# Performance work log

Hardware: AMD Instinct MI355X
Metric: run time of the kernel (lower is better)

Reference implementation:

```python
import jax, jax.numpy as jnp
import numpy as np

N = 30000      # nodes
E = 400000     # edges per sparse set / GAT graph
F_IN = 512     # num_features
NHID = 128     # nhid
H = 4          # GAT heads
NCLS = 10      # num_classes
NSETS = 5      # num_gat = (3**2-1)//2 + 1
EPS = 1e-5     # BatchNorm eps


def setup_inputs() -> dict:
    key = jax.random.key(0)
    ks = jax.random.split(key, 24)
    s_in = 1.0 / np.sqrt(F_IN)
    s_h = 1.0 / np.sqrt(NHID)
    s_hh = 1.0 / np.sqrt(H * NHID)
    inp = {
        "x": jax.random.normal(ks[0], (N, F_IN), jnp.float32),
        "edge_index": jax.random.randint(ks[1], (2, E), 0, N),
        "scatter_idx": jax.random.randint(ks[2], (NSETS, 2, E), 0, N),
        "scatter_w": jax.random.normal(ks[3], (NSETS, E), jnp.float32) * 0.1,
        "lin_in_W": jax.random.normal(ks[4], (F_IN, NHID), jnp.float32) * s_in,
        "lin_in_b": jnp.zeros((NHID,), jnp.float32),
        "gat_W": jax.random.normal(ks[5], (NSETS, NHID, H * NHID), jnp.float32) * s_h,
        "att_src": jax.random.normal(ks[6], (NSETS, H, NHID), jnp.float32) * s_h,
        "att_dst": jax.random.normal(ks[7], (NSETS, H, NHID), jnp.float32) * s_h,
        "gat_b": jnp.zeros((NSETS, H * NHID), jnp.float32),
        "mlp_W": jax.random.normal(ks[8], (NSETS, H * NHID, NHID), jnp.float32) * s_hh,
        "mlp_b": jnp.zeros((NSETS, NHID), jnp.float32),
        "bn_g": jnp.ones((NSETS, NHID), jnp.float32),
        "bn_b": jnp.zeros((NSETS, NHID), jnp.float32),
        "bn_m": jax.random.normal(ks[9], (NSETS, NHID), jnp.float32) * 0.1,
        "bn_v": jax.random.uniform(ks[10], (NSETS, NHID), jnp.float32) + 0.5,
        "bn0_g": jnp.ones((NHID,), jnp.float32),
        "bn0_b": jnp.zeros((NHID,), jnp.float32),
        "bn0_m": jax.random.normal(ks[11], (NHID,), jnp.float32) * 0.1,
        "bn0_v": jax.random.uniform(ks[12], (NHID,), jnp.float32) + 0.5,
        "out_W": jax.random.normal(ks[13], (NHID, NCLS), jnp.float32) * s_h,
        "out_b": jnp.zeros((NCLS,), jnp.float32),
    }
    return inp


def _forward(x, edge_index, scatter_idx, scatter_w, lin_in_W, lin_in_b,
             gat_W, att_src, att_dst, gat_b, mlp_W, mlp_b,
             bn_g, bn_b, bn_m, bn_v, bn0_g, bn0_b, bn0_m, bn0_v, out_W, out_b):
    # solo_pass: gather source features, weight by edge value, scatter-add at dest
    def sp(i, xx):
        msg = scatter_w[i][:, None] * xx[scatter_idx[i, 0]]          # [E, NHID]
        return jax.ops.segment_sum(msg, scatter_idx[i, 1], num_segments=N)

    h = x @ lin_in_W + lin_in_b                                       # [N, NHID]
    x0 = sp(0, h)
    xhs = [jnp.abs(sp(i, h)) for i in range(1, NSETS)]
    xs = [x0] + [sp(0, xh) for xh in xhs]

    # GATConv adds self-loops by default
    loops = jnp.arange(N)
    src = jnp.concatenate([edge_index[0], loops])
    dst = jnp.concatenate([edge_index[1], loops])

    def gat(i, xx):
        hh = (xx @ gat_W[i]).reshape(N, H, NHID)                      # [N,H,C]
        a_s = (hh * att_src[i]).sum(-1)                               # [N,H]
        a_d = (hh * att_dst[i]).sum(-1)                               # [N,H]
        e = jax.nn.leaky_relu(a_s[src] + a_d[dst], 0.2)               # [E+N,H]
        m = jax.ops.segment_max(e, dst, num_segments=N)
        ex = jnp.exp(e - m[dst])
        den = jax.ops.segment_sum(ex, dst, num_segments=N)
        alpha = ex / (den[dst] + 1e-16)                               # [E+N,H]
        out = jax.ops.segment_sum(alpha[:, :, None] * hh[src], dst, num_segments=N)
        return out.reshape(N, H * NHID) + gat_b[i]

    # Seq(ELU, Dropout(eval=no-op), Linear, BatchNorm1d(eval))
    def mlp(i, xx):
        z = jax.nn.elu(xx) @ mlp_W[i] + mlp_b[i]
        return (z - bn_m[i]) * jax.lax.rsqrt(bn_v[i] + EPS) * bn_g[i] + bn_b[i]

    outs = [mlp(i, gat(i, xs[i])) for i in range(NSETS)]
    x_stage2 = h + outs[0] + outs[1] + outs[2] + outs[3] + outs[4]

    z = (x_stage2 - bn0_m) * jax.lax.rsqrt(bn0_v + EPS) * bn0_g + bn0_b
    z = jax.nn.elu(z) @ out_W + out_b
    return jax.nn.log_softmax(z, axis=1)


def reference(x, edge_index, scatter_idx, scatter_w, lin_in_W, lin_in_b,
              gat_W, att_src, att_dst, gat_b, mlp_W, mlp_b,
              bn_g, bn_b, bn_m, bn_v, bn0_g, bn0_b, bn0_m, bn0_v, out_W, out_b):
    return _forward(x, edge_index, scatter_idx, scatter_w, lin_in_W, lin_in_b,
                    gat_W, att_src, att_dst, gat_b, mlp_W, mlp_b,
                    bn_g, bn_b, bn_m, bn_v, bn0_g, bn0_b, bn0_m, bn0_v, out_W, out_b)
```

## Files before the change

kernel.cpp:

```cpp
#include <hip/hip_runtime.h>
#include <cstdint>
#include <cstddef>

#define NN 30000
#define NE 400000
#define EG (NE + NN)
#define NSETS 5
#define NCLS 10
#define BN_EPS 1e-5f

#define NBKT 118
#define CHUNK 4096
#define NWG_SET 98
#define NWG_GAT 105
#define NWGMAX 105
#define NBLK_BIN (5 * NWG_SET + NWG_GAT)
#define NBLK_SORT (6 * NBKT)
#define LIN_B 469

typedef __bf16 bf16x8 __attribute__((ext_vector_type(8)));
typedef float  f32x4  __attribute__((ext_vector_type(4)));

constexpr size_t alg(size_t x) { return (x + 255) & ~size_t(255); }
constexpr size_t OFF_U1    = 0;
constexpr size_t OFF_HB    = OFF_U1   + alg((size_t)5 * NN * 128 * 2);
constexpr size_t OFF_X2    = OFF_HB   + alg((size_t)NN * 128 * 2);
constexpr size_t OFF_AGG   = OFF_X2   + alg((size_t)NN * 128 * 4);
constexpr size_t OFF_GOUT  = OFF_AGG  + alg((size_t)NN * 512 * 2);
constexpr size_t OFF_WT    = OFF_GOUT + alg((size_t)NN * 512 * 2);
constexpr size_t OFF_WATT  = OFF_WT   + alg((size_t)11 * 65536 * 2);
constexpr size_t OFF_OFF6  = OFF_WATT + alg((size_t)5 * 2 * 4 * 128 * 4);
constexpr size_t OFF_SPP   = OFF_OFF6 + alg((size_t)6 * (NN + 1) * 4);
constexpr size_t OFF_GSRC  = OFF_SPP  + alg((size_t)NSETS * NE * 8);
constexpr size_t OFF_CNT   = OFF_GSRC + alg((size_t)EG * 4);
constexpr size_t OFF_AS5   = OFF_CNT  + alg((size_t)12 * NN * 4);
constexpr size_t OFF_AD5   = OFF_AS5  + alg((size_t)5 * NN * 4 * 4);
constexpr size_t WS_NEED   = OFF_AD5  + alg((size_t)5 * NN * 4 * 4);

__device__ __forceinline__ float lrelu02(float v) { return v > 0.f ? v : 0.2f * v; }
__device__ __forceinline__ float eluf(float v)    { return v > 0.f ? v : __expf(v) - 1.f; }
__device__ __forceinline__ float bf2f(unsigned u) {
    union { unsigned i; float f; } c; c.i = u << 16; return c.f;
}
__device__ __forceinline__ unsigned short f2bf(float f) {
    union { float f; unsigned i; } c; c.f = f;
    unsigned u = c.i + 0x7FFFu + ((c.i >> 16) & 1u);
    return (unsigned short)(u >> 16);
}
__device__ __forceinline__ void gload_lds16(const void* g, void* l) {
    __builtin_amdgcn_global_load_lds(
        (const __attribute__((address_space(1))) void*)(uintptr_t)g,
        (__attribute__((address_space(3))) void*)(unsigned)(uintptr_t)l,
        16, 0, 0);
}

__device__ __forceinline__ void chunk_map(int blk, int& g, int& wg, int& e0, int& e1) {
    if (blk < 5 * NWG_SET) { g = blk / NWG_SET; wg = blk - g * NWG_SET; }
    else                   { g = 5;             wg = blk - 5 * NWG_SET; }
    e0 = wg * CHUNK;
    e1 = min(e0 + CHUNK, (g < 5) ? NE : EG);
}

#define PREP_CVX_B 1024
#define PREP_TRW_B 512
#define PREP_WAT_B 20
#define PREP_HIST_B NBLK_BIN
#define PREP_GRID (PREP_CVX_B + PREP_TRW_B + PREP_WAT_B + PREP_HIST_B)

__global__ void prep1(const int* __restrict__ scat_idx, const int* __restrict__ edge_ix,
                      int* __restrict__ bh,
                      const float* __restrict__ x, unsigned short* __restrict__ xb,
                      const float* __restrict__ lin_W, const float* __restrict__ gat_W,
                      const float* __restrict__ mlp_W,
                      unsigned short* __restrict__ linWT, unsigned short* __restrict__ gatWT,
                      unsigned short* __restrict__ mlpWT,
                      const float* __restrict__ att_src, const float* __restrict__ att_dst,
                      float* __restrict__ watt) {
    __shared__ int h[NBKT];
    const int b = blockIdx.x;
    if (b < PREP_CVX_B) {
        const int total = NN * 512 / 4;
        for (int i = b * 256 + threadIdx.x; i < total; i += PREP_CVX_B * 256) {
            float4 v = *(const float4*)(x + (size_t)i * 4);
            ushort4 o;
            o.x = f2bf(v.x); o.y = f2bf(v.y); o.z = f2bf(v.z); o.w = f2bf(v.w);
            *(ushort4*)(xb + (size_t)i * 4) = o;
        }
    } else if (b < PREP_CVX_B + PREP_TRW_B) {
        const int bb = b - PREP_CVX_B;
        const int total = 65536 + 2 * 327680;
        for (int i = bb * 256 + threadIdx.x; i < total; i += PREP_TRW_B * 256) {
            if (i < 65536) {
                int n = i >> 9, k = i & 511;
                linWT[i] = f2bf(lin_W[(size_t)k * 128 + n]);
            } else if (i < 65536 + 327680) {
                int li = i - 65536;
                int st = li >> 16, r = li & 65535;
                int n = r >> 7, k = r & 127;
                gatWT[li] = f2bf(gat_W[(size_t)st * 65536 + (size_t)k * 512 + n]);
            } else {
                int li = i - 65536 - 327680;
// ... 157 lines not shown
        int g, wg, e0, e1;
        chunk_map(blockIdx.x - LIN_B, g, wg, e0, e1);
        for (int i = t; i < NBKT; i += 256) {
            lpos[i] = pos[(size_t)(g * NBKT + i) * NWGMAX + wg];
            lcur[i] = 0;
        }
        __syncthreads();
        if (g < 5) {
            const int* si = scat_idx + (size_t)g * 2 * NE;
            const float* sw = scat_w + (size_t)g * NE;
            for (int e = e0 + t; e < e1; e += 256) {
                int src = si[e], d = si[NE + e];
                int r = atomicAdd(&lcur[d >> 8], 1);
                int2 pk; pk.x = src | (d << 15); pk.y = __float_as_int(sw[e]);
                stg_sp[(size_t)g * NE + lpos[d >> 8] + r] = pk;
            }
        } else {
            for (int e = e0 + t; e < e1; e += 256) {
                int src, d;
                if (e < NE) { src = edge_ix[e]; d = edge_ix[NE + e]; }
                else        { src = e - NE;     d = src; }
                int r = atomicAdd(&lcur[d >> 8], 1);
                stg_g[lpos[d >> 8] + r] = src | (d << 15);
            }
        }
    }
}

__global__ void __launch_bounds__(256) sortP(const int* __restrict__ bb,
                                             const int2* __restrict__ stg_sp, const int* __restrict__ stg_g,
                                             int2* __restrict__ spp, int* __restrict__ g_src,
                                             int* __restrict__ off6) {
    __shared__ int lcnt[256];
    __shared__ int loff[257];
    const int gb = blockIdx.x;
    const int g = gb / NBKT, bk = gb - g * NBKT;
    const int n0 = bk << 8;
    const int nlen = min(256, NN - n0);
    const int base = bb[g * 132 + bk];
    const int end  = bb[g * 132 + bk + 1];
    const int t = threadIdx.x;
    lcnt[t] = 0;
    __syncthreads();
    if (g < 5) {
        for (int j = base + t; j < end; j += 256)
            atomicAdd(&lcnt[((stg_sp[(size_t)g * NE + j].x >> 15) & 0x7fff) - n0], 1);
    } else {
        for (int j = base + t; j < end; j += 256)
            atomicAdd(&lcnt[((stg_g[j] >> 15) & 0x7fff) - n0], 1);
    }
    __syncthreads();
    int v = lcnt[t];
    __syncthreads();
    for (int d = 1; d < 256; d <<= 1) {
        int u = (t >= d) ? lcnt[t - d] : 0;
        __syncthreads();
        lcnt[t] += u;
        __syncthreads();
    }
    loff[t] = base + lcnt[t] - v;
    if (t == 255) loff[256] = base + lcnt[255];
    __syncthreads();
    if (t < nlen) off6[g * (NN + 1) + n0 + t] = loff[t];
    lcnt[t] = 0;
    __syncthreads();
    if (g < 5) {
        for (int j = base + t; j < end; j += 256) {
            int2 pk = stg_sp[(size_t)g * NE + j];
            int ln = ((pk.x >> 15) & 0x7fff) - n0;
            int p = loff[ln] + atomicAdd(&lcnt[ln], 1);
            int2 o; o.x = pk.x & 0x7fff; o.y = pk.y;
            spp[(size_t)g * NE + p] = o;
        }
    } else {
        for (int j = base + t; j < end; j += 256) {
            int w = stg_g[j];
            int ln = ((w >> 15) & 0x7fff) - n0;
            int p = loff[ln] + atomicAdd(&lcnt[ln], 1);
            g_src[p] = w & 0x7fff;
        }
    }
}

__global__ void __launch_bounds__(256) fusedGM(const unsigned short* __restrict__ agg,
                                               const unsigned short* __restrict__ gatWT,
                                               const unsigned short* __restrict__ mlpWT,
                                               const float* __restrict__ gat_b,
                                               const float* __restrict__ mlp_b,
                                               const float* __restrict__ bng, const float* __restrict__ bnb,
                                               const float* __restrict__ bnm, const float* __restrict__ bnv,
                                               float* __restrict__ x2) {
    __shared__ __align__(16) char U[49152];
    __shared__ __align__(16) char gtile[16384];
    const int t = threadIdx.x, wave = t >> 6, lane = t & 63;
    const int bm = blockIdx.x * 64;
    const int wr = (wave >> 1) * 32, wc = (wave & 1) * 64;
    const int l15 = lane & 15, l4 = lane >> 4;
    const int rsw = (l15 & 7) << 4;
    f32x4 acc2[2][4] = {};

    #pragma unroll
    for (int h = 0; h < 4; ++h) {
        stage64<64>(agg, 512, bm, NN - 1, h * 128,       U,         t);
        stage64<64>(agg, 512, bm, NN - 1, h * 128 + 64,  U + 8192,  t);
        stage64<128>(gatWT, 128, h * 128, 511, 0,        U + 16384, t);
        stage64<128>(gatWT, 128, h * 128, 511, 64,       U + 32768, t);
        __syncthreads();

        f32x4 a1[2][4] = {};
        #pragma unroll
        for (int ks = 0; ks < 4; ++ks) {
            const char* Asb = U + (ks >> 1) * 8192;
            const char* Bsb = U + 16384 + (ks >> 1) * 16384;
            const int koff = (ks & 1) * 64 + l4 * 16;
            bf16x8 af[2], bf[4];
            #pragma unroll
            for (int fm = 0; fm < 2; ++fm)
                af[fm] = *(const bf16x8*)(Asb + (wr + fm * 16 + l15) * 128 + (koff ^ rsw));
            #pragma unroll
            for (int fn = 0; fn < 4; ++fn)
                bf[fn] = *(const bf16x8*)(Bsb + (wc + fn * 16 + l15) * 128 + (koff ^ rsw));
            #pragma unroll
            for (int fm = 0; fm < 2; ++fm)
                #pragma unroll
                for (int fn = 0; fn < 4; ++fn)
                    a1[fm][fn] = __builtin_amdgcn_mfma_f32_16x16x32_bf16(af[fm], bf[fn], a1[fm][fn], 0, 0, 0);
        }
        __syncthreads();

        #pragma unroll
        for (int fn = 0; fn < 4; ++fn) {
            const int cc = wc + fn * 16 + l15;
            const float gb = gat_b[h * 128 + cc];
            #pragma unroll
            for (int fm = 0; fm < 2; ++fm) {
                #pragma unroll
                for (int rg = 0; rg < 4; ++rg) {
                    const int r = wr + fm * 16 + l4 * 4 + rg;
                    const unsigned short v = f2bf(eluf(a1[fm][fn][rg] + gb));
                    *(unsigned short*)(gtile + r * 256 + ((((cc >> 3) ^ (r & 7)) << 4) | ((cc & 7) << 1))) = v;
                }
            }
        }
        stage64<128>(mlpWT, 512, 0, 127, h * 128,      U,         t);
        stage64<128>(mlpWT, 512, 0, 127, h * 128 + 64, U + 16384, t);
        __syncthreads();

        #pragma unroll
        for (int ks = 0; ks < 4; ++ks) {
            const int s2 = ks >> 1, kk = ks & 1;
            const char* slab = U + s2 * 16384;
            bf16x8 af[2], bf[4];
            #pragma unroll
            for (int fm = 0; fm < 2; ++fm) {
                const int r2 = wr + fm * 16 + l15;
                const int chunk = (s2 * 8 + kk * 4 + l4) ^ (r2 & 7);
                af[fm] = *(const bf16x8*)(gtile + r2 * 256 + (chunk << 4));
            }
            const int koff = kk * 64 + l4 * 16;
            #pragma unroll
            for (int fn = 0; fn < 4; ++fn)
                bf[fn] = *(const bf16x8*)(slab + (wc + fn * 16 + l15) * 128 + (koff ^ rsw));
            #pragma unroll
            for (int fm = 0; fm < 2; ++fm)
                #pragma unroll
                for (int fn = 0; fn < 4; ++fn)
                    acc2[fm][fn] = __builtin_amdgcn_mfma_f32_16x16x32_bf16(af[fm], bf[fn], acc2[fm][fn], 0, 0, 0);
        }
        __syncthreads();
    }

    #pragma unroll
    for (int fn = 0; fn < 4; ++fn) {
        const int c = wc + fn * 16 + l15;
        const float sc = bng[c] * rsqrtf(bnv[c] + BN_EPS);
        const float sh = bnb[c] - bnm[c] * sc;
        const float mb = mlp_b[c];
        #pragma unroll
        for (int fm = 0; fm < 2; ++fm) {
            #pragma unroll
            for (int rg = 0; rg < 4; ++rg) {
                int r = bm + wr + fm * 16 + l4 * 4 + rg;
                if (r < NN)
                    x2[(size_t)r * 128 + c] += (acc2[fm][fn][rg] + mb) * sc + sh;
            }
        }
    }
}

__global__ void __launch_bounds__(256) sp_abs4(const int* __restrict__ off6,
                                               const int2* __restrict__ spp,
                                               const unsigned short* __restrict__ hb,
                                               unsigned short* __restrict__ tmp4) {
    const int y = blockIdx.y;
    const int* off = off6 + (y + 1) * (NN + 1);
    const int2* pk = spp + (size_t)(y + 1) * NE;
    unsigned short* out = tmp4 + (size_t)y * NN * 128;

    const int wid  = blockIdx.x * 4 + (threadIdx.x >> 6);
    const int lane = threadIdx.x & 63;
    const int co   = lane * 2;
    const int s0 = off[wid], s1 = off[wid + 1];
    float a0 = 0.f, a1 = 0.f;
    int j = s0;
    for (; j + 7 < s1; j += 8) {
        int2 e[8];
        unsigned v[8];
        #pragma unroll
        for (int q = 0; q < 8; ++q) e[q] = pk[j + q];
        #pragma unroll
        for (int q = 0; q < 8; ++q) v[q] = *(const unsigned*)(hb + (size_t)e[q].x * 128 + co);
        #pragma unroll
        for (int q = 0; q < 8; ++q) {
            float w = __int_as_float(e[q].y);
            a0 = fmaf(w, bf2f(v[q] & 0xffffu), a0);
            a1 = fmaf(w, bf2f(v[q] >> 16), a1);
        }
    }
    for (; j < s1; ++j) {
        int2 e = pk[j];
        float wj = __int_as_float(e.y);
        unsigned v = *(const unsigned*)(hb + (size_t)e.x * 128 + co);
        a0 = fmaf(wj, bf2f(v & 0xffffu), a0);
        a1 = fmaf(wj, bf2f(v >> 16), a1);
    }
    a0 = fabsf(a0); a1 = fabsf(a1);
    unsigned o = (unsigned)f2bf(a0) | ((unsigned)f2bf(a1) << 16);
    *(unsigned*)(out + (size_t)wid * 128 + co) = o;
}

__global__ void __launch_bounds__(256) sp_fused5(const int* __restrict__ off0,
                                                 const int2* __restrict__ spp0,
                                                 const unsigned short* __restrict__ hb,
                                                 const unsigned short* __restrict__ tmp4,
                                                 unsigned short* __restrict__ xcur5,
                                                 const float* __restrict__ watt,
                                                 float* __restrict__ as5,
                                                 float* __restrict__ ad5) {
    __shared__ float sWatt[5120];
    for (int i = threadIdx.x; i < 5120; i += 256) sWatt[i] = watt[i];
    __syncthreads();

    const int wid  = blockIdx.x * 4 + (threadIdx.x >> 6);
    const int lane = threadIdx.x & 63;
    const int co   = lane * 2;
    const int s0 = off0[wid], s1 = off0[wid + 1];
    const unsigned short* tbl[5] = {
        hb, tmp4, tmp4 + (size_t)1 * NN * 128, tmp4 + (size_t)2 * NN * 128, tmp4 + (size_t)3 * NN * 128 };

    float a[5][2] = {};
    int j = s0;
    for (; j + 3 < s1; j += 4) {
        int2 e0 = spp0[j], e1 = spp0[j + 1], e2 = spp0[j + 2], e3 = spp0[j + 3];
        size_t r0 = (size_t)e0.x * 128 + co, r1 = (size_t)e1.x * 128 + co;
        size_t r2 = (size_t)e2.x * 128 + co, r3 = (size_t)e3.x * 128 + co;
        unsigned v[5][4];
        #pragma unroll
        for (int y = 0; y < 5; ++y) {
            v[y][0] = *(const unsigned*)(tbl[y] + r0);
            v[y][1] = *(const unsigned*)(tbl[y] + r1);
            v[y][2] = *(const unsigned*)(tbl[y] + r2);
            v[y][3] = *(const unsigned*)(tbl[y] + r3);
        }
        float w0 = __int_as_float(e0.y), w1 = __int_as_float(e1.y);
        float w2 = __int_as_float(e2.y), w3 = __int_as_float(e3.y);
        #pragma unroll
        for (int y = 0; y < 5; ++y) {
            a[y][0] = fmaf(w0, bf2f(v[y][0] & 0xffffu), a[y][0]); a[y][1] = fmaf(w0, bf2f(v[y][0] >> 16), a[y][1]);
            a[y][0] = fmaf(w1, bf2f(v[y][1] & 0xffffu), a[y][0]); a[y][1] = fmaf(w1, bf2f(v[y][1] >> 16), a[y][1]);
            a[y][0] = fmaf(w2, bf2f(v[y][2] & 0xffffu), a[y][0]); a[y][1] = fmaf(w2, bf2f(v[y][2] >> 16), a[y][1]);
            a[y][0] = fmaf(w3, bf2f(v[y][3] & 0xffffu), a[y][0]); a[y][1] = fmaf(w3, bf2f(v[y][3] >> 16), a[y][1]);
        }
    }
    for (; j < s1; ++j) {
        int2 e = spp0[j];
        size_t r = (size_t)e.x * 128 + co;
        float wj = __int_as_float(e.y);
        #pragma unroll
        for (int y = 0; y < 5; ++y) {
            unsigned v = *(const unsigned*)(tbl[y] + r);
            a[y][0] = fmaf(wj, bf2f(v & 0xffffu), a[y][0]);
            a[y][1] = fmaf(wj, bf2f(v >> 16), a[y][1]);
        }
    }
    #pragma unroll
    for (int y = 0; y < 5; ++y) {
        unsigned o = (unsigned)f2bf(a[y][0]) | ((unsigned)f2bf(a[y][1]) << 16);
        *(unsigned*)(xcur5 + (size_t)y * NN * 128 + (size_t)wid * 128 + co) = o;
    }

    #pragma unroll
    for (int i = 0; i < 5; ++i) {
        #pragma unroll
        for (int h = 0; h < 4; ++h) {
            const float* wS = sWatt + ((i * 2 + 0) * 4 + h) * 128;
            const float* wD = sWatt + ((i * 2 + 1) * 4 + h) * 128;
            float ps = a[i][0] * wS[co] + a[i][1] * wS[co + 1];
            float pd = a[i][0] * wD[co] + a[i][1] * wD[co + 1];
            #pragma unroll
            for (int dd = 1; dd < 64; dd <<= 1) { ps += __shfl_xor(ps, dd); pd += __shfl_xor(pd, dd); }
            if (lane == 0) {
                as5[(size_t)i * NN * 4 + (size_t)wid * 4 + h] = ps;
                ad5[(size_t)i * NN * 4 + (size_t)wid * 4 + h] = pd;
            }
        }
    }
}

__device__ __forceinline__ void acc8(float* a, float al, uint4 v) {
    a[0] = fmaf(al, bf2f(v.x & 0xffffu), a[0]); a[1] = fmaf(al, bf2f(v.x >> 16), a[1]);
    a[2] = fmaf(al, bf2f(v.y & 0xffffu), a[2]); a[3] = fmaf(al, bf2f(v.y >> 16), a[3]);
    a[4] = fmaf(al, bf2f(v.z & 0xffffu), a[4]); a[5] = fmaf(al, bf2f(v.z >> 16), a[5]);
    a[6] = fmaf(al, bf2f(v.w & 0xffffu), a[6]); a[7] = fmaf(al, bf2f(v.w >> 16), a[7]);
}

__global__ void __launch_bounds__(256) gat_agg2(const int* __restrict__ goff, const int* __restrict__ gsrc,
                                                const float* __restrict__ as_, const float* __restrict__ ad_,
                                                const unsigned short* __restrict__ xcur,
                                                unsigned short* __restrict__ agg) {
    const int wid  = blockIdx.x * 4 + (threadIdx.x >> 6);
    const int lane = threadIdx.x & 63;
    const int hd   = lane >> 4;
    const int cl   = (lane & 15) * 8;
    const int s0 = goff[wid], s1 = goff[wid + 1];
    const float4 adv4 = *(const float4*)(ad_ + (size_t)wid * 4);

    float m[4] = {-1e30f, -1e30f, -1e30f, -1e30f};
    float s[4] = {0.f, 0.f, 0.f, 0.f};
    for (int j = s0 + lane; j < s1; j += 64) {
        const int si = gsrc[j];
        float4 av = *(const float4*)(as_ + (size_t)si * 4);
        float e[4] = {lrelu02(av.x + adv4.x), lrelu02(av.y + adv4.y),
                      lrelu02(av.z + adv4.z), lrelu02(av.w + adv4.w)};
        #pragma unroll
        for (int h = 0; h < 4; ++h) {
            if (e[h] > m[h]) { s[h] = s[h] * __expf(m[h] - e[h]) + 1.f; m[h] = e[h]; }
            else             { s[h] += __expf(e[h] - m[h]); }
        }
    }
    #pragma unroll
    for (int d = 1; d < 64; d <<= 1) {
        #pragma unroll
        for (int h = 0; h < 4; ++h) {
            float om = __shfl_xor(m[h], d);
            float os = __shfl_xor(s[h], d);
            float nm = fmaxf(m[h], om);
            s[h] = s[h] * __expf(m[h] - nm) + os * __expf(om - nm);
            m[h] = nm;
        }
    }
    const float advh = hd == 0 ? adv4.x : hd == 1 ? adv4.y : hd == 2 ? adv4.z : adv4.w;
    const float mv   = hd == 0 ? m[0]   : hd == 1 ? m[1]   : hd == 2 ? m[2]   : m[3];
    const float dv   = hd == 0 ? s[0]   : hd == 1 ? s[1]   : hd == 2 ? s[2]   : s[3];
    const float inv  = 1.f / (dv + 1e-16f);

    float ac[8] = {};
    int j = s0;
    for (; j + 3 < s1; j += 4) {
        int i0 = gsrc[j], i1 = gsrc[j + 1], i2 = gsrc[j + 2], i3 = gsrc[j + 3];
        float q0 = as_[(size_t)i0 * 4 + hd], q1 = as_[(size_t)i1 * 4 + hd];
        float q2 = as_[(size_t)i2 * 4 + hd], q3 = as_[(size_t)i3 * 4 + hd];
        uint4 v0 = *(const uint4*)(xcur + (size_t)i0 * 128 + cl);
        uint4 v1 = *(const uint4*)(xcur + (size_t)i1 * 128 + cl);
        uint4 v2 = *(const uint4*)(xcur + (size_t)i2 * 128 + cl);
        uint4 v3 = *(const uint4*)(xcur + (size_t)i3 * 128 + cl);
        float al0 = __expf(lrelu02(q0 + advh) - mv) * inv;
        float al1 = __expf(lrelu02(q1 + advh) - mv) * inv;
        float al2 = __expf(lrelu02(q2 + advh) - mv) * inv;
        float al3 = __expf(lrelu02(q3 + advh) - mv) * inv;
        acc8(ac, al0, v0); acc8(ac, al1, v1); acc8(ac, al2, v2); acc8(ac, al3, v3);
    }
    for (; j < s1; ++j) {
        int si = gsrc[j];
        float q = as_[(size_t)si * 4 + hd];
        uint4 v = *(const uint4*)(xcur + (size_t)si * 128 + cl);
        float al = __expf(lrelu02(q + advh) - mv) * inv;
        acc8(ac, al, v);
    }
    uint4 ov;
    ov.x = (unsigned)f2bf(ac[0]) | ((unsigned)f2bf(ac[1]) << 16);
    ov.y = (unsigned)f2bf(ac[2]) | ((unsigned)f2bf(ac[3]) << 16);
    ov.z = (unsigned)f2bf(ac[4]) | ((unsigned)f2bf(ac[5]) << 16);
    ov.w = (unsigned)f2bf(ac[6]) | ((unsigned)f2bf(ac[7]) << 16);
    *(uint4*)(agg + (size_t)wid * 512 + hd * 128 + cl) = ov;
}

__global__ void __launch_bounds__(256) final_out(const float* __restrict__ x2,
                                                 const float* __restrict__ bn0g, const float* __restrict__ bn0b,
                                                 const float* __restrict__ bn0m, const float* __restrict__ bn0v,
                                                 const float* __restrict__ outW, const float* __restrict__ outb,
                                                 float* __restrict__ out) {
    __shared__ float sW[128 * 12];
    __shared__ float sSc[128], sSh[128];
    for (int i = threadIdx.x; i < 1280; i += 256) {
        int r = i / 10, c = i - r * 10;
        sW[r * 12 + c] = outW[i];
    }
    if (threadIdx.x < 128) {
        int c = threadIdx.x;
        float sc = bn0g[c] * rsqrtf(bn0v[c] + BN_EPS);
        sSc[c] = sc;
        sSh[c] = bn0b[c] - bn0m[c] * sc;
    }
    __syncthreads();
    const int wid  = blockIdx.x * 4 + (threadIdx.x >> 6);
    const int lane = threadIdx.x & 63;
    const int c0 = lane * 2;
    float2 a = *(const float2*)(x2 + (size_t)wid * 128 + c0);
    float a0 = eluf(a.x * sSc[c0] + sSh[c0]);
    float a1 = eluf(a.y * sSc[c0 + 1] + sSh[c0 + 1]);
    float p[NCLS];
    #pragma unroll
    for (int j = 0; j < NCLS; ++j)
        p[j] = a0 * sW[c0 * 12 + j] + a1 * sW[(c0 + 1) * 12 + j];
    #pragma unroll
    for (int j = 0; j < NCLS; ++j) {
        float v = p[j];
        v += __shfl_xor(v, 1);  v += __shfl_xor(v, 2);  v += __shfl_xor(v, 4);
        v += __shfl_xor(v, 8);  v += __shfl_xor(v, 16); v += __shfl_xor(v, 32);
        p[j] = v;
    }
    float z[NCLS];
    #pragma unroll
    for (int j = 0; j < NCLS; ++j) z[j] = p[j] + outb[j];
    float m = z[0];
    #pragma unroll
    for (int j = 1; j < NCLS; ++j) m = fmaxf(m, z[j]);
    float ssum = 0.f;
    #pragma unroll
    for (int j = 0; j < NCLS; ++j) ssum += __expf(z[j] - m);
    float lse = m + __logf(ssum);
    #pragma unroll
    for (int j = 0; j < NCLS; ++j)
        if (lane == j) out[(size_t)wid * NCLS + j] = z[j] - lse;
}

extern "C" void kernel_launch(void* const* d_in, const int* in_sizes, int n_in,
                              void* d_out, int out_size, void* d_ws, size_t ws_size,
                              hipStream_t stream) {
    const float* x        = (const float*)d_in[0];
    const int*   edge_ix  = (const int*)  d_in[1];
    const int*   scat_idx = (const int*)  d_in[2];
    const float* scat_w   = (const float*)d_in[3];
    const float* lin_W    = (const float*)d_in[4];
    const float* lin_b    = (const float*)d_in[5];
    const float* gat_W    = (const float*)d_in[6];
    const float* att_src  = (const float*)d_in[7];
    const float* att_dst  = (const float*)d_in[8];
    const float* gat_b    = (const float*)d_in[9];
    const float* mlp_W    = (const float*)d_in[10];
    const float* mlp_b    = (const float*)d_in[11];
    const float* bn_g     = (const float*)d_in[12];
    const float* bn_b     = (const float*)d_in[13];
    const float* bn_m     = (const float*)d_in[14];
    const float* bn_v     = (const float*)d_in[15];
    const float* bn0_g    = (const float*)d_in[16];
    const float* bn0_b    = (const float*)d_in[17];
    const float* bn0_m    = (const float*)d_in[18];
    const float* bn0_v    = (const float*)d_in[19];
    const float* out_W    = (const float*)d_in[20];
    const float* out_b    = (const float*)d_in[21];
    float* out = (float*)d_out;

    char* ws = (char*)d_ws;
    unsigned short* xb    = (unsigned short*)(ws + OFF_U1);
    unsigned short* xcur5 = (unsigned short*)(ws + OFF_U1);
    unsigned short* hb    = (unsigned short*)(ws + OFF_HB);
    float*          x2    = (float*)(ws + OFF_X2);
    unsigned short* agg   = (unsigned short*)(ws + OFF_AGG);
    unsigned short* tmp4  = (unsigned short*)(ws + OFF_GOUT);
    int2*  stg_sp = (int2*)(ws + OFF_GOUT);
    int*   stg_g  = (int*)(ws + OFF_GOUT + (size_t)NSETS * NE * 8);
    unsigned short* wt    = (unsigned short*)(ws + OFF_WT);
    unsigned short* linWT = wt;
    unsigned short* gatWT = wt + 65536;
    unsigned short* mlpWT = wt + 65536 * 6;
    float* watt   = (float*)(ws + OFF_WATT);
    int*   off6   = (int*)(ws + OFF_OFF6);
    int2*  spp    = (int2*)(ws + OFF_SPP);
    int*   g_src  = (int*)(ws + OFF_GSRC);
    int*   bh     = (int*)(ws + OFF_CNT);
    int*   bb     = bh + NBLK_SORT * NWGMAX;
    float* as5    = (float*)(ws + OFF_AS5);
    float* ad5    = (float*)(ws + OFF_AD5);

    const dim3 b256(256);

    prep1<<<PREP_GRID, b256, 0, stream>>>(scat_idx, edge_ix, bh, x, xb,
                                          lin_W, gat_W, mlp_W, linWT, gatWT, mlpWT,
                                          att_src, att_dst, watt);
    bktscan<<<6, 128, 0, stream>>>(bh, bb, off6);
    wgscan<<<NBLK_SORT, 128, 0, stream>>>(bb, bh);
    binlin<<<LIN_B + NBLK_BIN, b256, 0, stream>>>(scat_idx, scat_w, edge_ix, bh, stg_sp, stg_g,
                                                  xb, linWT, lin_b, hb, x2);
    sortP<<<NBLK_SORT, b256, 0, stream>>>(bb, stg_sp, stg_g, spp, g_src, off6);

    sp_abs4<<<dim3(7500, 4), b256, 0, stream>>>(off6, spp, hb, tmp4);
    sp_fused5<<<7500, b256, 0, stream>>>(off6, spp, hb, tmp4, xcur5, watt, as5, ad5);

    for (int i = 0; i < NSETS; ++i) {
        gat_agg2<<<7500, b256, 0, stream>>>(off6 + 5 * (NN + 1), g_src,
                                            as5 + (size_t)i * NN * 4, ad5 + (size_t)i * NN * 4,
                                            xcur5 + (size_t)i * NN * 128, agg);
        fusedGM<<<469, b256, 0, stream>>>(agg, gatWT + (size_t)i * 65536, mlpWT + (size_t)i * 65536,
                                          gat_b + (size_t)i * 512, mlp_b + (size_t)i * 128,
                                          bn_g + (size_t)i * 128, bn_b + (size_t)i * 128,
                                          bn_m + (size_t)i * 128, bn_v + (size_t)i * 128, x2);
    }

    final_out<<<7500, b256, 0, stream>>>(x2, bn0_g, bn0_b, bn0_m, bn0_v, out_W, out_b, out);
}
```

Baseline: 665.9 us.

## Overlap GAT aggregation of set i with GEMM+MLP of set i-1 in one kernel

Adds a combined kernel that runs the dense GAT-projection+MLP+BN work for the previous set alongside the sparse attention aggregation for the current set, using double-buffered aggregation outputs. The GEMM body is restructured to use less LDS (a smaller A/B staging buffer with more syncs) so the gather blocks and matrix blocks can co-reside on the same compute units. The goal is to hide the memory-bound gather latency behind MFMA work and cut kernel launches. In exchange there are more barriers in the GEMM, and the block-type dispatch by blockIdx can make the two kinds of blocks compete for resources.

Result: slower. 936.5 us (+40.6%).

```diff
diff --git a/kernel.cpp b/kernel.cpp
--- a/kernel.cpp
+++ b/kernel.cpp
@@ -17,6 +17,8 @@
 #define NBLK_BIN (5 * NWG_SET + NWG_GAT)
 #define NBLK_SORT (6 * NBKT)
 #define LIN_B 469
+#define GM_B 469
+#define COMB_GRID (GM_B * 17)
 
 typedef __bf16 bf16x8 __attribute__((ext_vector_type(8)));
 typedef float  f32x4  __attribute__((ext_vector_type(4)));
@@ -340,231 +342,6 @@
     }
 }
 
-__global__ void __launch_bounds__(256) fusedGM(const unsigned short* __restrict__ agg,
-                                               const unsigned short* __restrict__ gatWT,
-                                               const unsigned short* __restrict__ mlpWT,
-                                               const float* __restrict__ gat_b,
-                                               const float* __restrict__ mlp_b,
-                                               const float* __restrict__ bng, const float* __restrict__ bnb,
-                                               const float* __restrict__ bnm, const float* __restrict__ bnv,
-                                               float* __restrict__ x2) {
-    __shared__ __align__(16) char U[49152];
-    __shared__ __align__(16) char gtile[16384];
-    const int t = threadIdx.x, wave = t >> 6, lane = t & 63;
-    const int bm = blockIdx.x * 64;
-    const int wr = (wave >> 1) * 32, wc = (wave & 1) * 64;
-    const int l15 = lane & 15, l4 = lane >> 4;
-    const int rsw = (l15 & 7) << 4;
-    f32x4 acc2[2][4] = {};
-
-    #pragma unroll
-    for (int h = 0; h < 4; ++h) {
-        stage64<64>(agg, 512, bm, NN - 1, h * 128,       U,         t);
-        stage64<64>(agg, 512, bm, NN - 1, h * 128 + 64,  U + 8192,  t);
-        stage64<128>(gatWT, 128, h * 128, 511, 0,        U + 16384, t);
-        stage64<128>(gatWT, 128, h * 128, 511, 64,       U + 32768, t);
-        __syncthreads();
-
-        f32x4 a1[2][4] = {};
-        #pragma unroll
-        for (int ks = 0; ks < 4; ++ks) {
-            const char* Asb = U + (ks >> 1) * 8192;
-            const char* Bsb = U + 16384 + (ks >> 1) * 16384;
-            const int koff = (ks & 1) * 64 + l4 * 16;
-            bf16x8 af[2], bf[4];
-            #pragma unroll
-            for (int fm = 0; fm < 2; ++fm)
-                af[fm] = *(const bf16x8*)(Asb + (wr + fm * 16 + l15) * 128 + (koff ^ rsw));
-            #pragma unroll
-            for (int fn = 0; fn < 4; ++fn)
-                bf[fn] = *(const bf16x8*)(Bsb + (wc + fn * 16 + l15) * 128 + (koff ^ rsw));
-            #pragma unroll
-            for (int fm = 0; fm < 2; ++fm)
-                #pragma unroll
-                for (int fn = 0; fn < 4; ++fn)
-                    a1[fm][fn] = __builtin_amdgcn_mfma_f32_16x16x32_bf16(af[fm], bf[fn], a1[fm][fn], 0, 0, 0);
-        }
-        __syncthreads();
-
-        #pragma unroll
-        for (int fn = 0; fn < 4; ++fn) {
-            const int cc = wc + fn * 16 + l15;
-            const float gb = gat_b[h * 128 + cc];
-            #pragma unroll
-            for (int fm = 0; fm < 2; ++fm) {
-                #pragma unroll
-                for (int rg = 0; rg < 4; ++rg) {
-                    const int r = wr + fm * 16 + l4 * 4 + rg;
-                    const unsigned short v = f2bf(eluf(a1[fm][fn][rg] + gb));
-                    *(unsigned short*)(gtile + r * 256 + ((((cc >> 3) ^ (r & 7)) << 4) | ((cc & 7) << 1))) = v;
-                }
-            }
-        }
-        stage64<128>(mlpWT, 512, 0, 127, h * 128,      U,         t);
-        stage64<128>(mlpWT, 512, 0, 127, h * 128 + 64, U + 16384, t);
-        __syncthreads();
-
-        #pragma unroll
-        for (int ks = 0; ks < 4; ++ks) {
-            const int s2 = ks >> 1, kk = ks & 1;
-            const char* slab = U + s2 * 16384;
-            bf16x8 af[2], bf[4];
-            #pragma unroll
-            for (int fm = 0; fm < 2; ++fm) {
-                const int r2 = wr + fm * 16 + l15;
-                const int chunk = (s2 * 8 + kk * 4 + l4) ^ (r2 & 7);
-                af[fm] = *(const bf16x8*)(gtile + r2 * 256 + (chunk << 4));
-            }
-            const int koff = kk * 64 + l4 * 16;
-            #pragma unroll
-            for (int fn = 0; fn < 4; ++fn)
-                bf[fn] = *(const bf16x8*)(slab + (wc + fn * 16 + l15) * 128 + (koff ^ rsw));
-            #pragma unroll
-            for (int fm = 0; fm < 2; ++fm)
-                #pragma unroll
-                for (int fn = 0; fn < 4; ++fn)
-                    acc2[fm][fn] = __builtin_amdgcn_mfma_f32_16x16x32_bf16(af[fm], bf[fn], acc2[fm][fn], 0, 0, 0);
-        }
-        __syncthreads();
-    }
-
-    #pragma unroll
-    for (int fn = 0; fn < 4; ++fn) {
-        const int c = wc + fn * 16 + l15;
-        const float sc = bng[c] * rsqrtf(bnv[c] + BN_EPS);
-        const float sh = bnb[c] - bnm[c] * sc;
-        const float mb = mlp_b[c];
-        #pragma unroll
-        for (int fm = 0; fm < 2; ++fm) {
-            #pragma unroll
-            for (int rg = 0; rg < 4; ++rg) {
-                int r = bm + wr + fm * 16 + l4 * 4 + rg;
-                if (r < NN)
-                    x2[(size_t)r * 128 + c] += (acc2[fm][fn][rg] + mb) * sc + sh;
-            }
-        }
-    }
-}
-
-__global__ void __launch_bounds__(256) sp_abs4(const int* __restrict__ off6,
-                                               const int2* __restrict__ spp,
-                                               const unsigned short* __restrict__ hb,
-                                               unsigned short* __restrict__ tmp4) {
-    const int y = blockIdx.y;
-    const int* off = off6 + (y + 1) * (NN + 1);
-    const int2* pk = spp + (size_t)(y + 1) * NE;
-    unsigned short* out = tmp4 + (size_t)y * NN * 128;
-
-    const int wid  = blockIdx.x * 4 + (threadIdx.x >> 6);
-    const int lane = threadIdx.x & 63;
-    const int co   = lane * 2;
-    const int s0 = off[wid], s1 = off[wid + 1];
-    float a0 = 0.f, a1 = 0.f;
-    int j = s0;
-    for (; j + 7 < s1; j += 8) {
-        int2 e[8];
-        unsigned v[8];
-        #pragma unroll
-        for (int q = 0; q < 8; ++q) e[q] = pk[j + q];
-        #pragma unroll
-        for (int q = 0; q < 8; ++q) v[q] = *(const unsigned*)(hb + (size_t)e[q].x * 128 + co);
-        #pragma unroll
-        for (int q = 0; q < 8; ++q) {
-            float w = __int_as_float(e[q].y);
-            a0 = fmaf(w, bf2f(v[q] & 0xffffu), a0);
-            a1 = fmaf(w, bf2f(v[q] >> 16), a1);
-        }
-    }
-    for (; j < s1; ++j) {
-        int2 e = pk[j];
-        float wj = __int_as_float(e.y);
-        unsigned v = *(const unsigned*)(hb + (size_t)e.x * 128 + co);
-        a0 = fmaf(wj, bf2f(v & 0xffffu), a0);
-        a1 = fmaf(wj, bf2f(v >> 16), a1);
-    }
-    a0 = fabsf(a0); a1 = fabsf(a1);
-    unsigned o = (unsigned)f2bf(a0) | ((unsigned)f2bf(a1) << 16);
-    *(unsigned*)(out + (size_t)wid * 128 + co) = o;
-}
-
-__global__ void __launch_bounds__(256) sp_fused5(const int* __restrict__ off0,
-                                                 const int2* __restrict__ spp0,
-                                                 const unsigned short* __restrict__ hb,
-                                                 const unsigned short* __restrict__ tmp4,
-                                                 unsigned short* __restrict__ xcur5,
-                                                 const float* __restrict__ watt,
-                                                 float* __restrict__ as5,
-                                                 float* __restrict__ ad5) {
-    __shared__ float sWatt[5120];
-    for (int i = threadIdx.x; i < 5120; i += 256) sWatt[i] = watt[i];
-    __syncthreads();
-
-    const int wid  = blockIdx.x * 4 + (threadIdx.x >> 6);
-    const int lane = threadIdx.x & 63;
-    const int co   = lane * 2;
-    const int s0 = off0[wid], s1 = off0[wid + 1];
-    const unsigned short* tbl[5] = {
-        hb, tmp4, tmp4 + (size_t)1 * NN * 128, tmp4 + (size_t)2 * NN * 128, tmp4 + (size_t)3 * NN * 128 };
-
-    float a[5][2] = {};
-    int j = s0;
-    for (; j + 3 < s1; j += 4) {
-        int2 e0 = spp0[j], e1 = spp0[j + 1], e2 = spp0[j + 2], e3 = spp0[j + 3];
-        size_t r0 = (size_t)e0.x * 128 + co, r1 = (size_t)e1.x * 128 + co;
-        size_t r2 = (size_t)e2.x * 128 + co, r3 = (size_t)e3.x * 128 + co;
-        unsigned v[5][4];
-        #pragma unroll
-        for (int y = 0; y < 5; ++y) {
-            v[y][0] = *(const unsigned*)(tbl[y] + r0);
-            v[y][1] = *(const unsigned*)(tbl[y] + r1);
-            v[y][2] = *(const unsigned*)(tbl[y] + r2);
-            v[y][3] = *(const unsigned*)(tbl[y] + r3);
-        }
-        float w0 = __int_as_float(e0.y), w1 = __int_as_float(e1.y);
-        float w2 = __int_as_float(e2.y), w3 = __int_as_float(e3.y);
-        #pragma unroll
-        for (int y = 0; y < 5; ++y) {
-            a[y][0] = fmaf(w0, bf2f(v[y][0] & 0xffffu), a[y][0]); a[y][1] = fmaf(w0, bf2f(v[y][0] >> 16), a[y][1]);
-            a[y][0] = fmaf(w1, bf2f(v[y][1] & 0xffffu), a[y][0]); a[y][1] = fmaf(w1, bf2f(v[y][1] >> 16), a[y][1]);
-            a[y][0] = fmaf(w2, bf2f(v[y][2] & 0xffffu), a[y][0]); a[y][1] = fmaf(w2, bf2f(v[y][2] >> 16), a[y][1]);
-            a[y][0] = fmaf(w3, bf2f(v[y][3] & 0xffffu), a[y][0]); a[y][1] = fmaf(w3, bf2f(v[y][3] >> 16), a[y][1]);
-        }
-    }
-    for (; j < s1; ++j) {
-        int2 e = spp0[j];
-        size_t r = (size_t)e.x * 128 + co;
-        float wj = __int_as_float(e.y);
-        #pragma unroll
-        for (int y = 0; y < 5; ++y) {
-            unsigned v = *(const unsigned*)(tbl[y] + r);
-            a[y][0] = fmaf(wj, bf2f(v & 0xffffu), a[y][0]);
-            a[y][1] = fmaf(wj, bf2f(v >> 16), a[y][1]);
-        }
-    }
-    #pragma unroll
-    for (int y = 0; y < 5; ++y) {
-        unsigned o = (unsigned)f2bf(a[y][0]) | ((unsigned)f2bf(a[y][1]) << 16);
-        *(unsigned*)(xcur5 + (size_t)y * NN * 128 + (size_t)wid * 128 + co) = o;
-    }
-
-    #pragma unroll
-    for (int i = 0; i < 5; ++i) {
-        #pragma unroll
-        for (int h = 0; h < 4; ++h) {
-            const float* wS = sWatt + ((i * 2 + 0) * 4 + h) * 128;
-            const float* wD = sWatt + ((i * 2 + 1) * 4 + h) * 128;
-            float ps = a[i][0] * wS[co] + a[i][1] * wS[co + 1];
-            float pd = a[i][0] * wD[co] + a[i][1] * wD[co + 1];
-            #pragma unroll
-            for (int dd = 1; dd < 64; dd <<= 1) { ps += __shfl_xor(ps, dd); pd += __shfl_xor(pd, dd); }
-            if (lane == 0) {
-                as5[(size_t)i * NN * 4 + (size_t)wid * 4 + h] = ps;
-                ad5[(size_t)i * NN * 4 + (size_t)wid * 4 + h] = pd;
-            }
-        }
-    }
-}
-
 __device__ __forceinline__ void acc8(float* a, float al, uint4 v) {
     a[0] = fmaf(al, bf2f(v.x & 0xffffu), a[0]); a[1] = fmaf(al, bf2f(v.x >> 16), a[1]);
     a[2] = fmaf(al, bf2f(v.y & 0xffffu), a[2]); a[3] = fmaf(al, bf2f(v.y >> 16), a[3]);
@@ -572,14 +349,13 @@
     a[6] = fmaf(al, bf2f(v.w & 0xffffu), a[6]); a[7] = fmaf(al, bf2f(v.w >> 16), a[7]);
 }
 
-__global__ void __launch_bounds__(256) gat_agg2(const int* __restrict__ goff, const int* __restrict__ gsrc,
-                                                const float* __restrict__ as_, const float* __restrict__ ad_,
-                                                const unsigned short* __restrict__ xcur,
-                                                unsigned short* __restrict__ agg) {
-    const int wid  = blockIdx.x * 4 + (threadIdx.x >> 6);
-    const int lane = threadIdx.x & 63;
-    const int hd   = lane >> 4;
-    const int cl   = (lane & 15) * 8;
+__device__ __forceinline__ void gat_body(int wid, int lane,
+                                         const int* __restrict__ goff, const int* __restrict__ gsrc,
+                                         const float* __restrict__ as_, const float* __restrict__ ad_,
+                                         const unsigned short* __restrict__ xcur,
+                                         unsigned short* __restrict__ agg) {
+    const int hd = lane >> 4;
+    const int cl = (lane & 15) * 8;
     const int s0 = goff[wid], s1 = goff[wid + 1];
     const float4 adv4 = *(const float4*)(ad_ + (size_t)wid * 4);
 
@@ -641,6 +417,274 @@
     ov.z = (unsigned)f2bf(ac[4]) | ((unsigned)f2bf(ac[5]) << 16);
     ov.w = (unsigned)f2bf(ac[6]) | ((unsigned)f2bf(ac[7]) << 16);
     *(uint4*)(agg + (size_t)wid * 512 + hd * 128 + cl) = ov;
+}
+
+__global__ void __launch_bounds__(256) gat_agg2(const int* __restrict__ goff, const int* __restrict__ gsrc,
+                                                const float* __restrict__ as_, const float* __restrict__ ad_,
+                                                const unsigned short* __restrict__ xcur,
+                                                unsigned short* __restrict__ agg) {
+    gat_body(blockIdx.x * 4 + (threadIdx.x >> 6), threadIdx.x & 63, goff, gsrc, as_, ad_, xcur, agg);
+}
+
+__device__ __forceinline__ void gm40_body(int bm, int t, char* shm,
+                                          const unsigned short* __restrict__ agg,
+                                          const unsigned short* __restrict__ gatWT,
+                                          const unsigned short* __restrict__ mlpWT,
+                                          const float* __restrict__ gat_b,
+                                          const float* __restrict__ mlp_b,
+                                          const float* __restrict__ bng, const float* __restrict__ bnb,
+                                          const float* __restrict__ bnm, const float* __restrict__ bnv,
+                                          float* __restrict__ x2) {
+    char* Ab = shm;
+    char* Bb = shm + 8192;
+    char* gt = shm + 8192 + 16384;
+    const int wave = t >> 6, lane = t & 63;
+    const int wr = (wave >> 1) * 32, wc = (wave & 1) * 64;
+    const int l15 = lane & 15, l4 = lane >> 4;
+    const int rsw = (l15 & 7) << 4;
+    f32x4 acc2[2][4] = {};
+
+    #pragma unroll
+    for (int h = 0; h < 4; ++h) {
+        f32x4 a1[2][4] = {};
+        #pragma unroll
+        for (int ks2 = 0; ks2 < 2; ++ks2) {
+            stage64<64>(agg, 512, bm, NN - 1, h * 128 + ks2 * 64, Ab, t);
+            stage64<128>(gatWT, 128, h * 128, 511, ks2 * 64, Bb, t);
+            __syncthreads();
+            #pragma unroll
+            for (int kk = 0; kk < 2; ++kk) {
+                bf16x8 af[2], bf[4];
+                const int koff = kk * 64 + l4 * 16;
+                #pragma unroll
+                for (int fm = 0; fm < 2; ++fm)
+                    af[fm] = *(const bf16x8*)(Ab + (wr + fm * 16 + l15) * 128 + (koff ^ rsw));
+                #pragma unroll
+                for (int fn = 0; fn < 4; ++fn)
+                    bf[fn] = *(const bf16x8*)(Bb + (wc + fn * 16 + l15) * 128 + (koff ^ rsw));
+                #pragma unroll
+                for (int fm = 0; fm < 2; ++fm)
+                    #pragma unroll
+                    for (int fn = 0; fn < 4; ++fn)
+                        a1[fm][fn] = __builtin_amdgcn_mfma_f32_16x16x32_bf16(af[fm], bf[fn], a1[fm][fn], 0, 0, 0);
+            }
+            __syncthreads();
+        }
+        #pragma unroll
+        for (int fn = 0; fn < 4; ++fn) {
+            const int cc = wc + fn * 16 + l15;
+            const float gb = gat_b[h * 128 + cc];
+            #pragma unroll
+            for (int fm = 0; fm < 2; ++fm) {
+                #pragma unroll
+                for (int rg = 0; rg < 4; ++rg) {
+                    const int r = wr + fm * 16 + l4 * 4 + rg;
+                    const unsigned short v = f2bf(eluf(a1[fm][fn][rg] + gb));
+                    *(unsigned short*)(gt + r * 256 + ((((cc >> 3) ^ (r & 7)) << 4) | ((cc & 7) << 1))) = v;
+                }
+            }
+        }
+        #pragma unroll
+        for (int ks2 = 0; ks2 < 2; ++ks2) {
+            stage64<128>(mlpWT, 512, 0, 127, h * 128 + ks2 * 64, Bb, t);
+            __syncthreads();
+            #pragma unroll
+            for (int kk = 0; kk < 2; ++kk) {
+                bf16x8 af[2], bf[4];
+                #pragma unroll
+                for (int fm = 0; fm < 2; ++fm) {
+                    const int r2 = wr + fm * 16 + l15;
+                    const int chunk = (ks2 * 8 + kk * 4 + l4) ^ (r2 & 7);
+                    af[fm] = *(const bf16x8*)(gt + r2 * 256 + (chunk << 4));
+                }
+                const int koff = kk * 64 + l4 * 16;
+                #pragma unroll
+                for (int fn = 0; fn < 4; ++fn)
+                    bf[fn] = *(const bf16x8*)(Bb + (wc + fn * 16 + l15) * 128 + (koff ^ rsw));
+                #pragma unroll
+                for (int fm = 0; fm < 2; ++fm)
+                    #pragma unroll
+                    for (int fn = 0; fn < 4; ++fn)
+                        acc2[fm][fn] = __builtin_amdgcn_mfma_f32_16x16x32_bf16(af[fm], bf[fn], acc2[fm][fn], 0, 0, 0);
+            }
+            __syncthreads();
+        }
+    }
+
+    #pragma unroll
+    for (int fn = 0; fn < 4; ++fn) {
+        const int c = wc + fn * 16 + l15;
+        const float sc = bng[c] * rsqrtf(bnv[c] + BN_EPS);
+        const float sh = bnb[c] - bnm[c] * sc;
+        const float mb = mlp_b[c];
+        #pragma unroll
+        for (int fm = 0; fm < 2; ++fm) {
+            #pragma unroll
+            for (int rg = 0; rg < 4; ++rg) {
+                int r = bm + wr + fm * 16 + l4 * 4 + rg;
+                if (r < NN)
+                    x2[(size_t)r * 128 + c] += (acc2[fm][fn][rg] + mb) * sc + sh;
+            }
+        }
+    }
+}
+
+__global__ void __launch_bounds__(256) fusedGM(const unsigned short* __restrict__ agg,
+                                               const unsigned short* __restrict__ gatWT,
+                                               const unsigned short* __restrict__ mlpWT,
+                                               const float* __restrict__ gat_b,
+                                               const float* __restrict__ mlp_b,
+                                               const float* __restrict__ bng, const float* __restrict__ bnb,
+                                               const float* __restrict__ bnm, const float* __restrict__ bnv,
+                                               float* __restrict__ x2) {
+    __shared__ __align__(16) char shm[40960];
+    gm40_body(blockIdx.x * 64, threadIdx.x, shm, agg, gatWT, mlpWT, gat_b, mlp_b,
+              bng, bnb, bnm, bnv, x2);
+}
+
+__global__ void __launch_bounds__(256) comb(const int* __restrict__ goff, const int* __restrict__ gsrc,
+                                            const float* __restrict__ as_g, const float* __restrict__ ad_g,
+                                            const unsigned short* __restrict__ xcur_g,
+                                            unsigned short* __restrict__ agg_w,
+                                            const unsigned short* __restrict__ agg_r,
+                                            const unsigned short* __restrict__ gatWT,
+                                            const unsigned short* __restrict__ mlpWT,
+                                            const float* __restrict__ gat_b,
+                                            const float* __restrict__ mlp_b,
+                                            const float* __restrict__ bng, const float* __restrict__ bnb,
+                                            const float* __restrict__ bnm, const float* __restrict__ bnv,
+                                            float* __restrict__ x2) {
+    __shared__ __align__(16) char shm[40960];
+    const int bid = blockIdx.x;
+    const int g17 = bid / 17, r17 = bid % 17;
+    if (r17 == 0) {
+        gm40_body(g17 * 64, threadIdx.x, shm, agg_r, gatWT, mlpWT, gat_b, mlp_b,
+                  bng, bnb, bnm, bnv, x2);
+    } else {
+        const int gatId = g17 * 16 + (r17 - 1);
+        if (gatId >= 7500) return;
+        gat_body(gatId * 4 + (threadIdx.x >> 6), threadIdx.x & 63,
+                 goff, gsrc, as_g, ad_g, xcur_g, agg_w);
+    }
+}
+
+__global__ void __launch_bounds__(256) sp_abs4(const int* __restrict__ off6,
+                                               const int2* __restrict__ spp,
+                                               const unsigned short* __restrict__ hb,
+                                               unsigned short* __restrict__ tmp4) {
+    const int y = blockIdx.y;
+    const int* off = off6 + (y + 1) * (NN + 1);
+    const int2* pk = spp + (size_t)(y + 1) * NE;
+    unsigned short* out = tmp4 + (size_t)y * NN * 128;
+
+    const int wid  = blockIdx.x * 4 + (threadIdx.x >> 6);
+    const int lane = threadIdx.x & 63;
+    const int co   = lane * 2;
+    const int s0 = off[wid], s1 = off[wid + 1];
+    float a0 = 0.f, a1 = 0.f;
+    int j = s0;
+    for (; j + 7 < s1; j += 8) {
+        int2 e[8];
+        unsigned v[8];
+        #pragma unroll
+        for (int q = 0; q < 8; ++q) e[q] = pk[j + q];
+        #pragma unroll
+        for (int q = 0; q < 8; ++q) v[q] = *(const unsigned*)(hb + (size_t)e[q].x * 128 + co);
+        #pragma unroll
+        for (int q = 0; q < 8; ++q) {
+            float w = __int_as_float(e[q].y);
+            a0 = fmaf(w, bf2f(v[q] & 0xffffu), a0);
+            a1 = fmaf(w, bf2f(v[q] >> 16), a1);
+        }
+    }
+    for (; j < s1; ++j) {
+        int2 e = pk[j];
+        float wj = __int_as_float(e.y);
+        unsigned v = *(const unsigned*)(hb + (size_t)e.x * 128 + co);
+        a0 = fmaf(wj, bf2f(v & 0xffffu), a0);
+        a1 = fmaf(wj, bf2f(v >> 16), a1);
+    }
+    a0 = fabsf(a0); a1 = fabsf(a1);
+    unsigned o = (unsigned)f2bf(a0) | ((unsigned)f2bf(a1) << 16);
+    *(unsigned*)(out + (size_t)wid * 128 + co) = o;
+}
+
+__global__ void __launch_bounds__(256) sp_fused5(const int* __restrict__ off0,
+                                                 const int2* __restrict__ spp0,
+                                                 const unsigned short* __restrict__ hb,
+                                                 const unsigned short* __restrict__ tmp4,
+                                                 unsigned short* __restrict__ xcur5,
+                                                 const float* __restrict__ watt,
+                                                 float* __restrict__ as5,
+                                                 float* __restrict__ ad5) {
+    __shared__ float sWatt[5120];
+    for (int i = threadIdx.x; i < 5120; i += 256) sWatt[i] = watt[i];
+    __syncthreads();
+
+    const int wid  = blockIdx.x * 4 + (threadIdx.x >> 6);
+    const int lane = threadIdx.x & 63;
+    const int co   = lane * 2;
+    const int s0 = off0[wid], s1 = off0[wid + 1];
+    const unsigned short* tbl[5] = {
+        hb, tmp4, tmp4 + (size_t)1 * NN * 128, tmp4 + (size_t)2 * NN * 128, tmp4 + (size_t)3 * NN * 128 };
+
+    float a[5][2] = {};
+    int j = s0;
+    for (; j + 3 < s1; j += 4) {
+        int2 e0 = spp0[j], e1 = spp0[j + 1], e2 = spp0[j + 2], e3 = spp0[j + 3];
+        size_t r0 = (size_t)e0.x * 128 + co, r1 = (size_t)e1.x * 128 + co;
+        size_t r2 = (size_t)e2.x * 128 + co, r3 = (size_t)e3.x * 128 + co;
+        unsigned v[5][4];
+        #pragma unroll
+        for (int y = 0; y < 5; ++y) {
+            v[y][0] = *(const unsigned*)(tbl[y] + r0);
+            v[y][1] = *(const unsigned*)(tbl[y] + r1);
+            v[y][2] = *(const unsigned*)(tbl[y] + r2);
+            v[y][3] = *(const unsigned*)(tbl[y] + r3);
+        }
+        float w0 = __int_as_float(e0.y), w1 = __int_as_float(e1.y);
+        float w2 = __int_as_float(e2.y), w3 = __int_as_float(e3.y);
+        #pragma unroll
+        for (int y = 0; y < 5; ++y) {
+            a[y][0] = fmaf(w0, bf2f(v[y][0] & 0xffffu), a[y][0]); a[y][1] = fmaf(w0, bf2f(v[y][0] >> 16), a[y][1]);
+            a[y][0] = fmaf(w1, bf2f(v[y][1] & 0xffffu), a[y][0]); a[y][1] = fmaf(w1, bf2f(v[y][1] >> 16), a[y][1]);
+            a[y][0] = fmaf(w2, bf2f(v[y][2] & 0xffffu), a[y][0]); a[y][1] = fmaf(w2, bf2f(v[y][2] >> 16), a[y][1]);
+            a[y][0] = fmaf(w3, bf2f(v[y][3] & 0xffffu), a[y][0]); a[y][1] = fmaf(w3, bf2f(v[y][3] >> 16), a[y][1]);
+        }
+    }
+    for (; j < s1; ++j) {
+        int2 e = spp0[j];
+        size_t r = (size_t)e.x * 128 + co;
+        float wj = __int_as_float(e.y);
+        #pragma unroll
+        for (int y = 0; y < 5; ++y) {
+            unsigned v = *(const unsigned*)(tbl[y] + r);
+            a[y][0] = fmaf(wj, bf2f(v & 0xffffu), a[y][0]);
+            a[y][1] = fmaf(wj, bf2f(v >> 16), a[y][1]);
+        }
+    }
+    #pragma unroll
+    for (int y = 0; y < 5; ++y) {
+        unsigned o = (unsigned)f2bf(a[y][0]) | ((unsigned)f2bf(a[y][1]) << 16);
+        *(unsigned*)(xcur5 + (size_t)y * NN * 128 + (size_t)wid * 128 + co) = o;
+    }
+
+    #pragma unroll
+    for (int i = 0; i < 5; ++i) {
+        #pragma unroll
+        for (int h = 0; h < 4; ++h) {
+            const float* wS = sWatt + ((i * 2 + 0) * 4 + h) * 128;
+            const float* wD = sWatt + ((i * 2 + 1) * 4 + h) * 128;
+            float ps = a[i][0] * wS[co] + a[i][1] * wS[co + 1];
+            float pd = a[i][0] * wD[co] + a[i][1] * wD[co + 1];
+            #pragma unroll
+            for (int dd = 1; dd < 64; dd <<= 1) { ps += __shfl_xor(ps, dd); pd += __shfl_xor(pd, dd); }
+            if (lane == 0) {
+                as5[(size_t)i * NN * 4 + (size_t)wid * 4 + h] = ps;
+                ad5[(size_t)i * NN * 4 + (size_t)wid * 4 + h] = pd;
+            }
+        }
+    }
 }
 
 __global__ void __launch_bounds__(256) final_out(const float* __restrict__ x2,
@@ -725,8 +769,9 @@
     unsigned short* xcur5 = (unsigned short*)(ws + OFF_U1);
     unsigned short* hb    = (unsigned short*)(ws + OFF_HB);
     float*          x2    = (float*)(ws + OFF_X2);
-    unsigned short* agg   = (unsigned short*)(ws + OFF_AGG);
+    unsigned short* aggA  = (unsigned short*)(ws + OFF_AGG);
     unsigned short* tmp4  = (unsigned short*)(ws + OFF_GOUT);
+    unsigned short* aggB  = (unsigned short*)(ws + OFF_GOUT);
     int2*  stg_sp = (int2*)(ws + OFF_GOUT);
     int*   stg_g  = (int*)(ws + OFF_GOUT + (size_t)NSETS * NE * 8);
     unsigned short* wt    = (unsigned short*)(ws + OFF_WT);
@@ -743,6 +788,7 @@
     float* ad5    = (float*)(ws + OFF_AD5);
 
     const dim3 b256(256);
+    const int* goff = off6 + 5 * (NN + 1);
 
     prep1<<<PREP_GRID, b256, 0, stream>>>(scat_idx, edge_ix, bh, x, xb,
                                           lin_W, gat_W, mlp_W, linWT, gatWT, mlpWT,
@@ -756,15 +802,23 @@
     sp_abs4<<<dim3(7500, 4), b256, 0, stream>>>(off6, spp, hb, tmp4);
     sp_fused5<<<7500, b256, 0, stream>>>(off6, spp, hb, tmp4, xcur5, watt, as5, ad5);
 
-    for (int i = 0; i < NSETS; ++i) {
-        gat_agg2<<<7500, b256, 0, stream>>>(off6 + 5 * (NN + 1), g_src,
-                                            as5 + (size_t)i * NN * 4, ad5 + (size_t)i * NN * 4,
-                                            xcur5 + (size_t)i * NN * 128, agg);
-        fusedGM<<<469, b256, 0, stream>>>(agg, gatWT + (size_t)i * 65536, mlpWT + (size_t)i * 65536,
-                                          gat_b + (size_t)i * 512, mlp_b + (size_t)i * 128,
-                                          bn_g + (size_t)i * 128, bn_b + (size_t)i * 128,
-                                          bn_m + (size_t)i * 128, bn_v + (size_t)i * 128, x2);
-    }
+    unsigned short* aggbuf[2] = { aggA, aggB };
+    gat_agg2<<<7500, b256, 0, stream>>>(goff, g_src, as5, ad5, xcur5, aggA);
+    for (int i = 1; i < NSETS; ++i) {
+        comb<<<COMB_GRID, b256, 0, stream>>>(
+            goff, g_src,
+            as5 + (size_t)i * NN * 4, ad5 + (size_t)i * NN * 4,
+            xcur5 + (size_t)i * NN * 128, aggbuf[i & 1],
+            aggbuf[(i - 1) & 1],
+            gatWT + (size_t)(i - 1) * 65536, mlpWT + (size_t)(i - 1) * 65536,
+            gat_b + (size_t)(i - 1) * 512, mlp_b + (size_t)(i - 1) * 128,
+            bn_g + (size_t)(i - 1) * 128, bn_b + (size_t)(i - 1) * 128,
+            bn_m + (size_t)(i - 1) * 128, bn_v + (size_t)(i - 1) * 128, x2);
+    }
+    fusedGM<<<GM_B, b256, 0, stream>>>(aggbuf[4 & 1], gatWT + (size_t)4 * 65536, mlpWT + (size_t)4 * 65536,
+                                       gat_b + (size_t)4 * 512, mlp_b + (size_t)4 * 128,
+                                       bn_g + (size_t)4 * 128, bn_b + (size_t)4 * 128,
+                                       bn_m + (size_t)4 * 128, bn_v + (size_t)4 * 128, x2);
 
     final_out<<<7500, b256, 0, stream>>>(x2, bn0_g, bn0_b, bn0_m, bn0_v, out_W, out_b, out);
 }
```
